# Optimization experiments

Hardware: AMD Instinct MI355X
Metric: run time of the kernel (lower is better)

## Reference

```python
import jax, jax.numpy as jnp
import numpy as np

N_POINTS = 1_200_000
MAX_POINTS = 10
MAX_VOXELS = 160_000


def setup_inputs() -> dict:
    key = jax.random.key(0)
    k1, k2, k3 = jax.random.split(key, 3)
    xy = jax.random.normal(k1, (N_POINTS, 2), dtype=jnp.float32) * 18.0
    z = jax.random.normal(k2, (N_POINTS, 1), dtype=jnp.float32) * 1.3 - 1.0
    feat = jax.random.normal(k3, (N_POINTS, 2), dtype=jnp.float32)
    points = jnp.concatenate([xy, z, feat], axis=1)
    return {
        'points': points,
        'voxel_size': jnp.array([0.075, 0.075, 0.2], dtype=jnp.float32),
        'coors_range': jnp.array([-54.0, -54.0, -5.0, 54.0, 54.0, 3.0], dtype=jnp.float32),
        'max_points': MAX_POINTS,
        'max_voxels': MAX_VOXELS,
    }


def reference(points, voxel_size, coors_range, max_points, max_voxels):
    """Deterministic hard voxelization (mmcv hard_voxelize semantics):
    - quantize points to integer voxel coords, drop out-of-range points
    - voxels are numbered in order of first point appearance
    - at most `max_points` points per voxel (first ones kept, in point order)
    - at most `max_voxels` voxels (first ones kept)
    Returns fixed-shape buffers plus voxel_num (original slices to voxel_num).
    """
    N, C = points.shape
    vmin = coors_range[:3]
    grid = jnp.round((coors_range[3:] - vmin) / voxel_size).astype(jnp.int32)  # (gx, gy, gz)

    c = jnp.floor((points[:, :3] - vmin) / voxel_size).astype(jnp.int32)  # [N,3] xyz voxel coords
    valid = jnp.all((c >= 0) & (c < grid), axis=1)

    gx, gy, gz = grid[0].astype(jnp.int64), grid[1].astype(jnp.int64), grid[2].astype(jnp.int64)
    lin = (c[:, 0].astype(jnp.int64) * gy + c[:, 1].astype(jnp.int64)) * gz + c[:, 2].astype(jnp.int64)
    total = gx * gy * gz
    lin = jnp.where(valid, lin, total)  # sentinel sorts last

    idx = jnp.arange(N, dtype=jnp.int64)
    # composite key: group by voxel, original point order within each voxel
    order = jnp.argsort(lin * N + idx)  # [N] stable grouping
    lin_s = lin[order]
    valid_s = valid[order]

    is_head = valid_s & jnp.concatenate([jnp.array([True]), lin_s[1:] != lin_s[:-1]])
    pos = jnp.arange(N, dtype=jnp.int32)
    head_pos = jax.lax.cummax(jnp.where(is_head, pos, -1))  # head position of each point's group
    slot = pos - head_pos  # slot within voxel (point order)

    # voxel id = rank of the group's first point among all group-head original indices
    head_orig = jnp.where(is_head, order, N)  # sentinel N for non-heads
    rank = jnp.argsort(jnp.argsort(head_orig)).astype(jnp.int32)  # heads -> 0..H-1 in first-occurrence order
    vox_id = rank[head_pos]  # [N] voxel id per sorted point

    keep = valid_s & (slot < max_points) & (vox_id < max_voxels)
    vid = jnp.where(keep, vox_id, max_voxels)  # dump row for dropped points
    slt = jnp.where(keep, slot, 0)
    vals = jnp.where(keep[:, None], points[order], 0.0)

    voxels = jnp.zeros((max_voxels + 1, max_points, C), dtype=points.dtype)
    voxels = voxels.at[vid, slt].add(vals)[:max_voxels]

    # coors in (z, y, x) order as in mmcv
    c_rev = c[order][:, ::-1]
    vid_h = jnp.where(is_head & (rank < max_voxels), rank, max_voxels)
    coors = jnp.zeros((max_voxels + 1, 3), dtype=jnp.int32)
    coors = coors.at[vid_h].set(jnp.where((vid_h < max_voxels)[:, None], c_rev, 0))[:max_voxels]

    cnt_idx = jnp.where(valid_s & (vox_id < max_voxels), vox_id, max_voxels)
    counts = jnp.zeros((max_voxels + 1,), dtype=jnp.int32).at[cnt_idx].add(1)[:max_voxels]
    num_points_per_voxel = jnp.minimum(counts, max_points)

    voxel_num = jnp.minimum(is_head.sum(dtype=jnp.int32), max_voxels)
    return voxels, coors, num_points_per_voxel, voxel_num
```

## Files before the change

kernel.cpp:

```cpp
#include <hip/hip_runtime.h>
#include <cstdint>

static constexpr int C     = 5;
static constexpr int MAXP  = 10;
static constexpr int MAXV  = 160000;
static constexpr int BLK   = 256;
static constexpr int RB    = 2048;
static constexpr int BCAP  = 1024;
static constexpr int EPT   = 8;
static constexpr int ELEMS = BLK * EPT;

static constexpr int VOX_OFF = 0;
static constexpr int CO_OFF  = MAXV * MAXP * C;
static constexpr int NPV_OFF = CO_OFF + MAXV * 3;
static constexpr int VN_OFF  = NPV_OFF + MAXV;

typedef unsigned long long u64;
static constexpr u64 BYTEMUL = 0x0101010101010101ull;

__device__ __forceinline__ int hashb(int k) {
    return (int)(((uint32_t)k * 2654435761u) >> 21);
}

__global__ void vx_prep(const float* __restrict__ pts, const float* __restrict__ vsz,
                        const float* __restrict__ crg, int* __restrict__ key0,
                        int* __restrict__ hist, u64* __restrict__ flags8,
                        float* __restrict__ out, int NP, int NP8) {
    __shared__ int sh[RB];
    int t = threadIdx.x, b = blockIdx.x;
    for (int d = t; d < RB; d += BLK) sh[d] = 0;
    float vx = vsz[0], vy = vsz[1], vz = vsz[2];
    float x0 = crg[0], y0 = crg[1], z0 = crg[2];
    int gx = (int)rintf((crg[3] - x0) / vx);
    int gy = (int)rintf((crg[4] - y0) / vy);
    int gz = (int)rintf((crg[5] - z0) / vz);
    __syncthreads();
    int base = b * ELEMS;
    #pragma unroll
    for (int r = 0; r < EPT; r++) {
        int i = base + r * BLK + t;
        if (i < NP) {
            float px = pts[i * C], py = pts[i * C + 1], pz = pts[i * C + 2];
            int cx = (int)floorf((px - x0) / vx);
            int cy = (int)floorf((py - y0) / vy);
            int cz = (int)floorf((pz - z0) / vz);
            bool valid = (cx >= 0) & (cx < gx) & (cy >= 0) & (cy < gy) & (cz >= 0) & (cz < gz);
            int k = (cx * gy + cy) * gz + cz;
            key0[i] = valid ? k : -1;
            if (valid) atomicAdd(&sh[hashb(k)], 1);
        }
    }
    __syncthreads();
    for (int d = t; d < RB; d += BLK) hist[b * RB + d] = sh[d];
    int tid = b * BLK + t, nth = gridDim.x * BLK;
    float4* out4 = (float4*)out;
    const float4 z4 = make_float4(0.f, 0.f, 0.f, 0.f);
    for (int i = tid; i < VN_OFF / 4; i += nth) out4[i] = z4;
    for (int i = tid; i < NP8; i += nth) flags8[i] = 0ull;
}

__global__ void vx_scanw(int* __restrict__ hist, int* __restrict__ dtot, int NB) {
    int t = threadIdx.x;
    int lane = t & 63;
    int d = blockIdx.x * 4 + (t >> 6);
    int carry = 0;
    for (int base = 0; base < NB; base += 64) {
        int b = base + lane;
        int v = (b < NB) ? hist[b * RB + d] : 0;
        int x = v;
        #pragma unroll
        for (int o = 1; o < 64; o <<= 1) {
            int y = __shfl_up(x, o, 64);
            if (lane >= o) x += y;
        }
        if (b < NB) hist[b * RB + d] = carry + x - v;
        carry += __shfl(x, 63, 64);
    }
    if (lane == 0) dtot[d] = carry;
}

__global__ void vx_scat(const int* __restrict__ key0, const int* __restrict__ hist,
                        const int* __restrict__ dtot, u64* __restrict__ pairA, int NP) {
    __shared__ int cnt[RB];
    int t = threadIdx.x, b = blockIdx.x;
    int lane = t & 63;
    if (t < 64) {
        int loc[32]; int run = 0;
        #pragma unroll
        for (int j = 0; j < 32; j++) { loc[j] = run; run += dtot[t * 32 + j]; }
        int tot = run;
        for (int o = 1; o < 64; o <<= 1) {
            int x = __shfl_up(tot, o, 64);
            if (lane >= o) tot += x;
        }
        int excl = tot - run;
        #pragma unroll
        for (int j = 0; j < 32; j++) cnt[t * 32 + j] = excl + loc[j];
    }
    __syncthreads();
    for (int d = t; d < RB; d += BLK) cnt[d] += hist[b * RB + d];
    __syncthreads();
    int base = b * ELEMS;
    #pragma unroll
    for (int r = 0; r < EPT; r++) {
        int i = base + r * BLK + t;
        if (i < NP) {
            int k = key0[i];
            if (k >= 0) {
                int pos = atomicAdd(&cnt[hashb(k)], 1);
                pairA[pos] = ((u64)(uint32_t)k << 32) | (uint32_t)i;
            }
        }
    }
}

__global__ void __launch_bounds__(512) vx_bsort(u64* __restrict__ pairA,
                                                const int* __restrict__ dtot,
                                                u64* __restrict__ flags8) {
    __shared__ u64 sp[BCAP];
    __shared__ int sb[2];
    int t = threadIdx.x, d = blockIdx.x;
    if (t < 64) {
        int acc = 0;
        for (int j = t; j < d; j += 64) acc += dtot[j];
        #pragma unroll
        for (int o = 32; o > 0; o >>= 1) acc += __shfl_down(acc, o, 64);
        if (t == 0) { sb[0] = acc; sb[1] = dtot[d]; }
    }
    __syncthreads();
    int start = sb[0], size = sb[1];
    if (size <= 0) return;
    if (size > BCAP) size = BCAP;
    for (int i = t; i < BCAP; i += 512) sp[i] = (i < size) ? pairA[start + i] : ~0ull;
    __syncthreads();
    for (int k2 = 2; k2 <= BCAP; k2 <<= 1) {
        for (int j = k2 >> 1; j > 0; j >>= 1) {
            int lo = t & (j - 1);
            int i  = ((t ^ lo) << 1) | lo;
            int ix = i | j;
            u64 a = sp[i], c = sp[ix];
            bool up = (i & k2) == 0;
            if ((a > c) == up) { sp[i] = c; sp[ix] = a; }
            __syncthreads();
        }
    }
    unsigned char* flags = (unsigned char*)flags8;
    for (int i = t; i < size; i += 512) {
        u64 p = sp[i];
        pairA[start + i] = p;
        bool head = (i == 0) || ((p >> 32) != (sp[i - 1] >> 32));
        if (head) flags[(uint32_t)(p & 0xFFFFFFFFull)] = 1;
    }
}

__global__ void vx_wpA(const u64* __restrict__ flags8, int* __restrict__ wsum, int NP8) {
    __shared__ int s[BLK];
    int t = threadIdx.x, i = blockIdx.x * BLK + t;
    u64 wv = (i < NP8) ? flags8[i] : 0ull;
    s[t] = (int)((wv * BYTEMUL) >> 56);
    __syncthreads();
    for (int o = BLK / 2; o > 0; o >>= 1) { if (t < o) s[t] += s[t + o]; __syncthreads(); }
    if (t == 0) wsum[blockIdx.x] = s[0];
}

__global__ void vx_wp2(const u64* __restrict__ flags8, const int* __restrict__ wsum,
                       int* __restrict__ wpfx, float* __restrict__ out_vnum, int NP8) {
    __shared__ int s[BLK];
    __shared__ int eS;
    int t = threadIdx.x, b = blockIdx.x;
    if (t < 64) {
        int acc = 0;
        for (int base = 0; base < b; base += 64) {
            int idx = base + t;
            int v = (idx < b) ? wsum[idx] : 0;
            #pragma unroll
            for (int o = 32; o > 0; o >>= 1) v += __shfl_down(v, o, 64);
            acc += v;
        }
        if (t == 0) eS = acc;
    }
    int i = b * BLK + t;
    u64 wv = (i < NP8) ? flags8[i] : 0ull;
    int v = (int)((wv * BYTEMUL) >> 56);
    s[t] = v;
    __syncthreads();
    for (int o = 1; o < BLK; o <<= 1) {
        int x = (t >= o) ? s[t - o] : 0; __syncthreads();
        s[t] += x; __syncthreads();
    }
    if (i < NP8) wpfx[i] = eS + s[t] - v;
    if (b == gridDim.x - 1 && t == BLK - 1) {
        int G = eS + s[t];
        out_vnum[0] = (float)(G < MAXV ? G : MAXV);
    }
}

__device__ __forceinline__ int vox_rank(const u64* flags8, const int* wpfx, int io) {
    int w = io >> 3, b8 = io & 7;
    u64 below = flags8[w] & ((1ull << (8 * b8)) - 1ull);
    return wpfx[w] + (int)((below * BYTEMUL) >> 56);
}

__global__ void vx_emit(const u64* __restrict__ pairA, const int* __restrict__ dtot,
                        const u64* __restrict__ flags8, const int* __restrict__ wpfx,
                        const float* __restrict__ pts, const float* __restrict__ vsz,
                        const float* __restrict__ crg, float* __restrict__ out) {
    __shared__ u64 sp[BCAP];
    __shared__ int gpos[BCAP + 1];
    __shared__ int s[BLK];
    __shared__ int sb[2];
    int t = threadIdx.x, d = blockIdx.x;
    if (t < 64) {
        int acc = 0;
        for (int j = t; j < d; j += 64) acc += dtot[j];
        #pragma unroll
        for (int o = 32; o > 0; o >>= 1) acc += __shfl_down(acc, o, 64);
        if (t == 0) { sb[0] = acc; sb[1] = dtot[d]; }
    }
    __syncthreads();
    int start = sb[0], size = sb[1];
    if (size <= 0) return;
    if (size > BCAP) size = BCAP;
    for (int i = t; i < size; i += BLK) sp[i] = pairA[start + i];
    __syncthreads();
    const int EL = BCAP / BLK;
    int i0 = t * EL;
    unsigned hbits = 0; int hcnt = 0;
    #pragma unroll
    for (int r = 0; r < EL; r++) {
        int i = i0 + r;
        if (i < size) {
            int k = (int)(sp[i] >> 32);
            int h = (i == 0) || (k != (int)(sp[i - 1] >> 32));
            hbits |= (unsigned)h << r;
            hcnt += h;
        }
    }
    s[t] = hcnt;
    __syncthreads();
    for (int o = 1; o < BLK; o <<= 1) {
        int x = (t >= o) ? s[t - o] : 0; __syncthreads();
        s[t] += x; __syncthreads();
    }
    int gbase = s[t] - hcnt;
    {
        int g = gbase;
        #pragma unroll
        for (int r = 0; r < EL; r++)
            if ((hbits >> r) & 1) gpos[g++] = i0 + r;
    }
    int NG = s[BLK - 1];
    if (t == 0) gpos[NG] = size;
    __syncthreads();
    int gyd = (int)rintf((crg[4] - crg[1]) / vsz[1]);
    int gzd = (int)rintf((crg[5] - crg[2]) / vsz[2]);
    int gg = gbase - 1;
    int cgg = -2, cvid = 0, cp0 = 0, cp1 = 0;
    #pragma unroll
    for (int r = 0; r < EL; r++) {
        int i = i0 + r;
        if (i >= size) break;
        int h = (hbits >> r) & 1;
        gg += h;
        u64 p = sp[i];
        int k = (int)(p >> 32);
        if (gg != cgg) {
            cgg = gg;
            cp0 = gpos[gg];
            cp1 = gpos[gg + 1];
            cvid = vox_rank(flags8, wpfx, (int)(sp[cp0] & 0xFFFFFFFFull));
        }
        if (cvid >= MAXV) continue;
        if (h) {
            int cz = k % gzd; int rr = k / gzd; int cy = rr % gyd; int cx = rr / gyd;
            out[CO_OFF + cvid * 3 + 0] = (float)cz;
            out[CO_OFF + cvid * 3 + 1] = (float)cy;
            out[CO_OFF + cvid * 3 + 2] = (float)cx;
            int gsz = cp1 - cp0;
            out[NPV_OFF + cvid] = (float)(gsz < MAXP ? gsz : MAXP);
        }
        int slot = i - cp0;
        if (slot >= MAXP) continue;
        int io = (int)(p & 0xFFFFFFFFull);
        const float* src = pts + io * C;
        float* dst = out + (cvid * MAXP + slot) * C;
        dst[0] = src[0]; dst[1] = src[1]; dst[2] = src[2]; dst[3] = src[3]; dst[4] = src[4];
    }
}

extern "C" void kernel_launch(void* const* d_in, const int* in_sizes, int n_in,
                              void* d_out, int out_size, void* d_ws, size_t ws_size,
                              hipStream_t stream) {
    if (!d_out || !d_ws || n_in < 3) return;
    const float* pts = (const float*)d_in[0];
    const float* vsz = (const float*)d_in[1];
    const float* crg = (const float*)d_in[2];
    if (!pts || !vsz || !crg) return;
    const int NP  = in_sizes[0] / C;
    if (NP <= 0) return;
    const int NB  = (NP + ELEMS - 1) / ELEMS;
    const int NP8 = (NP + 7) / 8;
    const int NWB = (NP8 + BLK - 1) / BLK;

    size_t need = (size_t)NP * 8ull
                + (size_t)NP * 4ull
                + (size_t)RB * NB * 4ull
                + (size_t)RB * 4ull
                + (size_t)NP8 * 8ull
                + (size_t)NP8 * 4ull
                + (size_t)NWB * 4ull + 64ull;
    if (ws_size < need) return;
    if ((size_t)out_size < (size_t)VN_OFF + 1) return;

    u64* pairA  = (u64*)d_ws;
    int* key0   = (int*)(pairA + NP);
    int* hist   = key0 + NP;
    int* dtot   = hist + (size_t)RB * NB;
    u64* flags8 = (u64*)(dtot + RB);
    int* wpfx   = (int*)(flags8 + NP8);
    int* wsum   = wpfx + NP8;
    float* out  = (float*)d_out;

    vx_prep<<<NB, BLK, 0, stream>>>(pts, vsz, crg, key0, hist, flags8, out, NP, NP8);
    vx_scanw<<<RB / 4, BLK, 0, stream>>>(hist, dtot, NB);
    vx_scat<<<NB, BLK, 0, stream>>>(key0, hist, dtot, pairA, NP);
    vx_bsort<<<RB, 512, 0, stream>>>(pairA, dtot, flags8);
    vx_wpA<<<NWB, BLK, 0, stream>>>(flags8, wsum, NP8);
    vx_wp2<<<NWB, BLK, 0, stream>>>(flags8, wsum, wpfx, out + VN_OFF, NP8);
    vx_emit<<<RB, BLK, 0, stream>>>(pairA, dtot, flags8, wpfx, pts, vsz, crg, out);
}
```

Baseline: 204.0 us.

## Do per-bucket bitonic sort in registers with wave shuffles

Measured after the change: 207.6 us. No clear change (+1.8%).

```diff
diff --git a/kernel.cpp b/kernel.cpp
--- a/kernel.cpp
+++ b/kernel.cpp
@@ -131,19 +131,43 @@
     int start = sb[0], size = sb[1];
     if (size <= 0) return;
     if (size > BCAP) size = BCAP;
-    for (int i = t; i < BCAP; i += 512) sp[i] = (i < size) ? pairA[start + i] : ~0ull;
-    __syncthreads();
+    u64 v0 = (t < size) ? pairA[start + t] : ~0ull;
+    u64 v1 = (t + 512 < size) ? pairA[start + 512 + t] : ~0ull;
     for (int k2 = 2; k2 <= BCAP; k2 <<= 1) {
-        for (int j = k2 >> 1; j > 0; j >>= 1) {
-            int lo = t & (j - 1);
-            int i  = ((t ^ lo) << 1) | lo;
-            int ix = i | j;
-            u64 a = sp[i], c = sp[ix];
-            bool up = (i & k2) == 0;
-            if ((a > c) == up) { sp[i] = c; sp[ix] = a; }
-            __syncthreads();
-        }
-    }
+        bool up0 = ((t & k2) == 0);
+        bool up1 = (((t + 512) & k2) == 0);
+        for (int j = k2 >> 1; j >= 64; j >>= 1) {
+            if (j == 512) {
+                u64 mn = v0 < v1 ? v0 : v1, mx = v0 < v1 ? v1 : v0;
+                v0 = up0 ? mn : mx;
+                v1 = up1 ? mx : mn;
+            } else {
+                __syncthreads();
+                sp[t] = v0; sp[t + 512] = v1;
+                __syncthreads();
+                u64 p0 = sp[t ^ j];
+                u64 p1 = sp[(t ^ j) + 512];
+                bool l = (t & j) == 0;
+                u64 mn0 = v0 < p0 ? v0 : p0, mx0 = v0 < p0 ? p0 : v0;
+                v0 = (l == up0) ? mn0 : mx0;
+                u64 mn1 = v1 < p1 ? v1 : p1, mx1 = v1 < p1 ? p1 : v1;
+                v1 = (l == up1) ? mn1 : mx1;
+            }
+        }
+        int jt = (k2 >> 1) < 32 ? (k2 >> 1) : 32;
+        for (int j = jt; j >= 1; j >>= 1) {
+            u64 p0 = __shfl_xor(v0, j, 64);
+            u64 p1 = __shfl_xor(v1, j, 64);
+            bool l = (t & j) == 0;
+            u64 mn0 = v0 < p0 ? v0 : p0, mx0 = v0 < p0 ? p0 : v0;
+            v0 = (l == up0) ? mn0 : mx0;
+            u64 mn1 = v1 < p1 ? v1 : p1, mx1 = v1 < p1 ? p1 : v1;
+            v1 = (l == up1) ? mn1 : mx1;
+        }
+    }
+    __syncthreads();
+    sp[t] = v0; sp[t + 512] = v1;
+    __syncthreads();
     unsigned char* flags = (unsigned char*)flags8;
     for (int i = t; i < size; i += 512) {
         u64 p = sp[i];
```

## Replace per-bucket bitonic sort with shared-memory hash grouping and rank placement

Applied to the files above, without the earlier changes.

Measured after the change: 180.2 us. 11.7% less time.

```diff
diff --git a/kernel.cpp b/kernel.cpp
--- a/kernel.cpp
+++ b/kernel.cpp
@@ -114,10 +114,14 @@
     }
 }
 
-__global__ void __launch_bounds__(512) vx_bsort(u64* __restrict__ pairA,
+__global__ void __launch_bounds__(512) vx_group(u64* __restrict__ pairA,
                                                 const int* __restrict__ dtot,
                                                 u64* __restrict__ flags8) {
-    __shared__ u64 sp[BCAP];
+    __shared__ int htab[BCAP];
+    __shared__ int cnt[BCAP];
+    __shared__ int seg[BCAP];
+    __shared__ u64 sq[BCAP];
+    __shared__ int swp[8];
     __shared__ int sb[2];
     int t = threadIdx.x, d = blockIdx.x;
     if (t < 64) {
@@ -127,29 +131,75 @@
         for (int o = 32; o > 0; o >>= 1) acc += __shfl_down(acc, o, 64);
         if (t == 0) { sb[0] = acc; sb[1] = dtot[d]; }
     }
+    for (int i = t; i < BCAP; i += 512) { htab[i] = -1; cnt[i] = 0; }
     __syncthreads();
     int start = sb[0], size = sb[1];
     if (size <= 0) return;
     if (size > BCAP) size = BCAP;
-    for (int i = t; i < BCAP; i += 512) sp[i] = (i < size) ? pairA[start + i] : ~0ull;
-    __syncthreads();
-    for (int k2 = 2; k2 <= BCAP; k2 <<= 1) {
-        for (int j = k2 >> 1; j > 0; j >>= 1) {
-            int lo = t & (j - 1);
-            int i  = ((t ^ lo) << 1) | lo;
-            int ix = i | j;
-            u64 a = sp[i], c = sp[ix];
-            bool up = (i & k2) == 0;
-            if ((a > c) == up) { sp[i] = c; sp[ix] = a; }
-            __syncthreads();
-        }
-    }
+    bool a0 = t < size, a1 = t + 512 < size;
+    u64 e0 = a0 ? pairA[start + t] : 0;
+    u64 e1 = a1 ? pairA[start + 512 + t] : 0;
+    int k0 = (int)(e0 >> 32), k1 = (int)(e1 >> 32);
+    int s0 = 0, s1 = 0;
+    if (a0) {
+        s0 = (int)(((uint32_t)k0 * 0x85EBCA77u) >> 22);
+        for (int it = 0; it < BCAP; ++it) {
+            int old = atomicCAS(&htab[s0], -1, k0);
+            if (old == -1 || old == k0) break;
+            s0 = (s0 + 1) & (BCAP - 1);
+        }
+        atomicAdd(&cnt[s0], 1);
+    }
+    if (a1) {
+        s1 = (int)(((uint32_t)k1 * 0x85EBCA77u) >> 22);
+        for (int it = 0; it < BCAP; ++it) {
+            int old = atomicCAS(&htab[s1], -1, k1);
+            if (old == -1 || old == k1) break;
+            s1 = (s1 + 1) & (BCAP - 1);
+        }
+        atomicAdd(&cnt[s1], 1);
+    }
+    __syncthreads();
+    int c0 = cnt[2 * t], c1 = cnt[2 * t + 1];
+    int v = c0 + c1;
+    int lane = t & 63, wv = t >> 6;
+    int x = v;
+    #pragma unroll
+    for (int o = 1; o < 64; o <<= 1) {
+        int y = __shfl_up(x, o, 64);
+        if (lane >= o) x += y;
+    }
+    if (lane == 63) swp[wv] = x;
+    for (int i = t; i < BCAP; i += 512) htab[i] = 0;
+    __syncthreads();
+    if (t == 0) {
+        int acc = 0;
+        #pragma unroll
+        for (int j = 0; j < 8; j++) { int tmp = swp[j]; swp[j] = acc; acc += tmp; }
+    }
+    __syncthreads();
+    int excl = swp[wv] + x - v;
+    seg[2 * t] = excl;
+    seg[2 * t + 1] = excl + c0;
+    __syncthreads();
+    int st0 = 0, cn0 = 0, st1 = 0, cn1 = 0;
+    if (a0) { st0 = seg[s0]; cn0 = cnt[s0]; sq[st0 + atomicAdd(&htab[s0], 1)] = e0; }
+    if (a1) { st1 = seg[s1]; cn1 = cnt[s1]; sq[st1 + atomicAdd(&htab[s1], 1)] = e1; }
+    __syncthreads();
     unsigned char* flags = (unsigned char*)flags8;
-    for (int i = t; i < size; i += 512) {
-        u64 p = sp[i];
-        pairA[start + i] = p;
-        bool head = (i == 0) || ((p >> 32) != (sp[i - 1] >> 32));
-        if (head) flags[(uint32_t)(p & 0xFFFFFFFFull)] = 1;
+    if (a0) {
+        uint32_t my = (uint32_t)e0;
+        int r = 0;
+        for (int q = st0; q < st0 + cn0; q++) r += ((uint32_t)sq[q] < my);
+        pairA[start + st0 + r] = e0;
+        if (r == 0) flags[my] = 1;
+    }
+    if (a1) {
+        uint32_t my = (uint32_t)e1;
+        int r = 0;
+        for (int q = st1; q < st1 + cn1; q++) r += ((uint32_t)sq[q] < my);
+        pairA[start + st1 + r] = e1;
+        if (r == 0) flags[my] = 1;
     }
 }
 
@@ -324,7 +374,7 @@
     vx_prep<<<NB, BLK, 0, stream>>>(pts, vsz, crg, key0, hist, flags8, out, NP, NP8);
     vx_scanw<<<RB / 4, BLK, 0, stream>>>(hist, dtot, NB);
     vx_scat<<<NB, BLK, 0, stream>>>(key0, hist, dtot, pairA, NP);
-    vx_bsort<<<RB, 512, 0, stream>>>(pairA, dtot, flags8);
+    vx_group<<<RB, 512, 0, stream>>>(pairA, dtot, flags8);
     vx_wpA<<<NWB, BLK, 0, stream>>>(flags8, wsum, NP8);
     vx_wp2<<<NWB, BLK, 0, stream>>>(flags8, wsum, wpfx, out + VN_OFF, NP8);
     vx_emit<<<RB, BLK, 0, stream>>>(pairA, dtot, flags8, wpfx, pts, vsz, crg, out);
```
